# Performance work log

Hardware: AMD Instinct MI355X
Metric: run time of the kernel (lower is better)

The kernel has to match this reference:

```python
import jax, jax.numpy as jnp
import numpy as np

D_MODEL = 1024
N_HEAD = 16
D_HEAD = D_MODEL // N_HEAD
B, S = 4, 2048


def setup_inputs() -> dict:
    key = jax.random.key(0)
    ks = jax.random.split(key, 10)
    def xavier(k, shape):
        fan_in, fan_out = shape[1], shape[0]
        limit = np.sqrt(6.0 / (fan_in + fan_out))
        return jax.random.uniform(k, shape, jnp.float32, -limit, limit)
    x = jax.random.normal(ks[0], (B, S, D_MODEL), jnp.float32)
    mask = jnp.tril(jnp.ones((S, S), jnp.int32))[None, None]  # causal [1,1,S,S]
    return {
        "x": x,
        "Wq": xavier(ks[1], (D_MODEL, D_MODEL)), "bq": jnp.zeros((D_MODEL,), jnp.float32),
        "Wk": xavier(ks[2], (D_MODEL, D_MODEL)), "bk": jnp.zeros((D_MODEL,), jnp.float32),
        "Wv": xavier(ks[3], (D_MODEL, D_MODEL)), "bv": jnp.zeros((D_MODEL,), jnp.float32),
        "Wo": xavier(ks[4], (D_MODEL, D_MODEL)), "bo": jnp.zeros((D_MODEL,), jnp.float32),
        "mask": mask,
    }


def reference(x, Wq, bq, Wk, bk, Wv, bv, Wo, bo, mask):
    b, s, d = x.shape
    # Linear layers use y = x @ W.T + b (torch convention)
    def proj(W, bias):
        y = jnp.einsum('bsd,ed->bse', x, W) + bias
        return y.reshape(b, s, N_HEAD, D_HEAD).transpose(0, 2, 1, 3)  # [B,H,S,Dh]
    q = proj(Wq, bq)
    k = proj(Wk, bk)
    v = proj(Wv, bv)
    scores = jnp.einsum('bhqd,bhkd->bhqk', q, k) / jnp.sqrt(jnp.float32(D_HEAD))
    scores = jnp.where(mask == 0, jnp.float32(-1e9), scores)
    attn = jax.nn.softmax(scores, axis=-1)  # dropout is identity at eval
    context = jnp.einsum('bhqk,bhkd->bhqd', attn, v)
    context = context.transpose(0, 2, 1, 3).reshape(b, s, d)
    return jnp.einsum('bsd,ed->bse', context, Wo) + bo
```

## Files before the change

### kernel.cpp

```cpp
#include <hip/hip_runtime.h>
#include <stdint.h>

#define D_MODEL 1024
#define NHEAD   16
#define DHEAD   64
#define BATCH   4
#define SEQ     2048
#define MTOT    (BATCH*SEQ)

typedef __attribute__((ext_vector_type(4))) float f32x4;
typedef __attribute__((ext_vector_type(8))) short bf16x8;

typedef __attribute__((address_space(3))) uint32_t lds_u32;
typedef const __attribute__((address_space(1))) uint32_t glb_u32;

__device__ static inline void gload_lds16(const void* g, void* l) {
    __builtin_amdgcn_global_load_lds((glb_u32*)g, (lds_u32*)l, 16, 0, 0);
}

__device__ static inline ushort f2bf(float f) {
    uint32_t u = __builtin_bit_cast(uint32_t, f);
    u += 0x7fffu + ((u >> 16) & 1u);
    return (ushort)(u >> 16);
}

__device__ static inline float exp2_fast(float x) {
    float r; asm("v_exp_f32 %0, %1" : "=v"(r) : "v"(x)); return r;
}
__device__ static inline uint32_t cvt_pk_bf16(float a, float b) {
    uint32_t r;
    asm("v_cvt_pk_bf16_f32 %0, %1, %2" : "=v"(r) : "v"(a), "v"(b));
    return r;
}

__global__ __launch_bounds__(256) void convert_kernel(
    const float4* __restrict__ x,
    const float4* __restrict__ wq, const float4* __restrict__ wk,
    const float4* __restrict__ wv, const float4* __restrict__ wo,
    ushort4* __restrict__ xb, ushort4* __restrict__ wb)
{
    const int NX4 = (MTOT * D_MODEL) / 4;
    const int NW4 = (D_MODEL * D_MODEL) / 4;
    const int TOT = NX4 + 4 * NW4;
    for (int i = blockIdx.x * blockDim.x + threadIdx.x; i < TOT;
         i += gridDim.x * blockDim.x) {
        float4 v; ushort4* dst;
        if (i < NX4) { v = x[i]; dst = &xb[i]; }
        else {
            int j = i - NX4;
            int w = j >> 18;
            int r = j & (NW4 - 1);
            const float4* s = (w == 0) ? wq : (w == 1) ? wk : (w == 2) ? wv : wo;
            v = s[r]; dst = &wb[(size_t)w * NW4 + r];
        }
        ushort4 o;
        o.x = f2bf(v.x); o.y = f2bf(v.y); o.z = f2bf(v.z); o.w = f2bf(v.w);
        *dst = o;
    }
}


#define GSWZ(r) ((((r) >> 2) ^ (r)) & 3)

#define GEMM_PIPE_BODY(APTR, BPTR)                                          \
    __shared__ __align__(16) ushort S[4 * 2 * 4096]; \
    const int tid = threadIdx.x;                                            \
    const int w = tid >> 6, l = tid & 63, lo = l & 15, hi = l >> 4;         \
    const int wr = w >> 1, wc = w & 1;                                      \
    const int srow = l >> 2, gg = l & 3;                                    \
    const int r0 = w * 16 + srow, r1 = 64 + w * 16 + srow;                  \
    const int q0 = gg ^ GSWZ(r0), q1 = gg ^ GSWZ(r1);                       \
    const ushort* aS0 = (APTR) + (size_t)(m0 + r0) * 1024 + q0 * 8;         \
    const ushort* aS1 = (APTR) + (size_t)(m0 + r1) * 1024 + q1 * 8;         \
    const ushort* bS0 = (BPTR) + (size_t)(n0 + r0) * 1024 + q0 * 8;         \
    const ushort* bS1 = (BPTR) + (size_t)(n0 + r1) * 1024 + q1 * 8;         \
    const int ldsA0 = (w * 16) * 32, ldsA1 = (64 + w * 16) * 32;            \
    int offA[4], offB[4];                                                   \
    _Pragma("unroll")                                                       \
    for (int mi = 0; mi < 4; ++mi) {                                        \
        const int rA = wr * 64 + mi * 16 + lo;                              \
        offA[mi] = rA * 64 + ((hi ^ GSWZ(rA)) << 4);                        \
        const int rB = wc * 64 + mi * 16 + lo;                              \
        offB[mi] = rB * 64 + ((hi ^ GSWZ(rB)) << 4);                        \
    }                                                                       \
    f32x4 acc[4][4] = {};                                                   \
    auto stage = [&](int st, int t) {                                       \
        ushort* b = &S[st * 8192];                                          \
        const int ko = t * 32;                                              \
        gload_lds16(aS0 + ko, b + ldsA0);                                   \
        gload_lds16(aS1 + ko, b + ldsA1);                                   \
        gload_lds16(bS0 + ko, b + 4096 + ldsA0);                            \
        gload_lds16(bS1 + ko, b + 4096 + ldsA1);                            \
    };                                                                      \
    stage(0, 0); stage(1, 1); stage(2, 2);                                  \
    asm volatile("s_waitcnt vmcnt(8)" ::: "memory");                        \
    __builtin_amdgcn_s_barrier();                                           \
    __builtin_amdgcn_sched_barrier(0);                                      \
    int st = 0;                                                             \
    for (int t = 0; t < 32; ++t) {                                          \
        if (t + 3 < 32) stage((st + 3) & 3, t + 3);                         \
        const char* base = (const char*)&S[st * 8192];                      \
        bf16x8 af[4], bfr[4];                                               \
        _Pragma("unroll")                                                   \
        for (int mi = 0; mi < 4; ++mi) {                                    \
            af[mi]  = *(const bf16x8*)(base + offA[mi]);                    \
            bfr[mi] = *(const bf16x8*)(base + 8192 + offB[mi]);             \
        }                                                                   \
        asm volatile("s_waitcnt lgkmcnt(0)" ::: "memory");                  \
        __builtin_amdgcn_sched_barrier(0);                                  \
        __builtin_amdgcn_s_setprio(1);                                      \
        _Pragma("unroll")                                                   \
        for (int mi = 0; mi < 4; ++mi)                                      \
            _Pragma("unroll")                                               \
            for (int ni = 0; ni < 4; ++ni)                                  \
                acc[mi][ni] = __builtin_amdgcn_mfma_f32_16x16x32_bf16(      \
                    af[mi], bfr[ni], acc[mi][ni], 0, 0, 0);                 \
        __builtin_amdgcn_s_setprio(0);                                      \
        if (t + 3 < 32)      { asm volatile("s_waitcnt vmcnt(8)" ::: "memory"); } \
        else if (t == 29)    { asm volatile("s_waitcnt vmcnt(4)" ::: "memory"); } \
        else if (t == 30)    { asm volatile("s_waitcnt vmcnt(0)" ::: "memory"); } \
        __builtin_amdgcn_s_barrier();                                       \
        __builtin_amdgcn_sched_barrier(0);                                  \
        st = (st + 1) & 3;                                                  \
    }

__global__ __launch_bounds__(256) void gemm_qkv(
    const ushort* __restrict__ A,
    const ushort* __restrict__ W3,
    const float* __restrict__ bq, const float* __restrict__ bk,
    const float* __restrict__ bv,
    ushort* __restrict__ Qb, ushort* __restrict__ Kb, ushort* __restrict__ Vtb,
    float qscale)
{
    const int id = blockIdx.x;
    const int mb = ((id & 7) << 3) | ((id >> 3) & 7);
    const int nb = id >> 6;
    const int m0 = mb * 128, n0 = nb * 128;

    GEMM_PIPE_BODY(A, W3)

    const int region = nb >> 3;
    const float scale = (region == 0) ? qscale : 1.0f;
    const float* bias = (region == 0) ? bq : (region == 1) ? bk : bv;
    ushort* outQK = (region == 0) ? Qb : Kb;

#pragma unroll
    for (int mi = 0; mi < 4; ++mi) {
#pragma unroll
        for (int ni = 0; ni < 4; ++ni) {
            const int gj  = n0 + wc * 64 + ni * 16 + lo;
            const int lcl = gj & 1023;
            const int h = lcl >> 6, dh = lcl & 63;
            const float bj = bias[lcl];
            if (region < 2) {
#pragma unroll
                for (int r = 0; r < 4; ++r) {
                    const int gi = m0 + wr * 64 + mi * 16 + hi * 4 + r;
                    const int b = gi >> 11, s = gi & (SEQ - 1);
                    outQK[(((size_t)(b * NHEAD + h)) * SEQ + s) * DHEAD + dh] =
                        f2bf((acc[mi][ni][r] + bj) * scale);
                }
            } else {
                const int gi0 = m0 + wr * 64 + mi * 16 + hi * 4;
                const int b = gi0 >> 11, s = gi0 & (SEQ - 1);
                ushort4 o4;
                o4.x = f2bf(acc[mi][ni][0] + bj);
                o4.y = f2bf(acc[mi][ni][1] + bj);
                o4.z = f2bf(acc[mi][ni][2] + bj);
                o4.w = f2bf(acc[mi][ni][3] + bj);
                *(ushort4*)&Vtb[(((size_t)(b * NHEAD + h)) * DHEAD + dh) * SEQ + s] = o4;
            }
        }
    }
}

__global__ __launch_bounds__(256) void gemm_out(
    const ushort* __restrict__ A,
    const ushort* __restrict__ W,
    const float*  __restrict__ bias,
    float* __restrict__ out)
{
    const int id = blockIdx.x;
    const int mb = ((id & 7) << 3) | ((id >> 3) & 7);
    const int nb = id >> 6;
    const int m0 = mb * 128, n0 = nb * 128;

    GEMM_PIPE_BODY(A, W)

#pragma unroll
    for (int mi = 0; mi < 4; ++mi)
#pragma unroll
        for (int ni = 0; ni < 4; ++ni) {
            const int gj = n0 + wc * 64 + ni * 16 + lo;
            const float bj = bias[gj];
#pragma unroll
            for (int r = 0; r < 4; ++r) {
                const int gi = m0 + wr * 64 + mi * 16 + hi * 4 + r;
                out[(size_t)gi * D_MODEL + gj] = acc[mi][ni][r] + bj;
            }
        }
}

__global__ __launch_bounds__(256) void attn_kernel(
    const ushort* __restrict__ Q, const ushort* __restrict__ K,
    const ushort* __restrict__ Vt, ushort* __restrict__ ctx)
{
    __shared__ __align__(16) ushort Ks[64 * 64];
    __shared__ __align__(16) ushort Vs[64 * 64];
    __shared__ __align__(16) ushort Pq[4 * 32 * 64];

    const int tid = threadIdx.x;
    const int w = tid >> 6, l = tid & 63, lo = l & 15, hi = l >> 4;
    const int sw = lo & 7;

    const int fid = blockIdx.x;
    const int xcd = fid & 7;
    const int u = fid >> 3;
    const int g = xcd * 8 + (u & 7);
    const int b = g >> 4, h = g & 15;
    const int j = u >> 3;
    const size_t base = (size_t)(b * NHEAD + h) * SEQ * DHEAD;

    const int krow = tid >> 3;
    const int kcol = (tid & 7) * 8;
    char* PqW = (char*)&Pq[w * 2048];

    for (int pass = 0; pass < 2; ++pass) {
        const int qt = pass ? (15 - j) : j;
        const int q0 = qt << 7;
        const int qw0 = q0 + w * 32;

        bf16x8 qf[2][2];
#pragma unroll
        for (int mi = 0; mi < 2; ++mi)
#pragma unroll
            for (int ks = 0; ks < 2; ++ks)
                qf[mi][ks] = *(const bf16x8*)&Q[base +
                    (size_t)(qw0 + mi * 16 + lo) * DHEAD + ks * 32 + hi * 8];

        f32x4 o[2][4] = {};
        float mrow[2] = {-1e30f, -1e30f}, lrow[2] = {0.f, 0.f};

        const int ntiles = (q0 + 128) >> 6;

        bf16x8 kregA[2], vregA[2], kregB[2], vregB[2];
#pragma unroll
        for (int c = 0; c < 2; ++c) {
            kregA[c] = *(const bf16x8*)&K[base + (size_t)(c * 32 + krow) * DHEAD + kcol];
            vregA[c] = *(const bf16x8*)&Vt[base + (size_t)(c * 32 + krow) * SEQ + kcol];
            kregB[c] = *(const bf16x8*)&K[base + (size_t)(64 + c * 32 + krow) * DHEAD + kcol];
            vregB[c] = *(const bf16x8*)&Vt[base + (size_t)(c * 32 + krow) * SEQ + 64 + kcol];
        }

        auto tile_body = [&](int t, bf16x8 (&KR)[2], bf16x8 (&VR)[2]) {
            const int kv0 = t << 6;
            __syncthreads();
#pragma unroll
            for (int c = 0; c < 2; ++c) {
                const int row = c * 32 + krow;
                const int g16 = (tid & 7) ^ (row & 7);
                *(bf16x8*)((char*)Ks + row * 128 + (g16 << 4)) = KR[c];
                *(bf16x8*)((char*)Vs + row * 128 + (g16 << 4)) = VR[c];
            }
            __syncthreads();
            if (t + 2 < ntiles) {
                const int nv0 = kv0 + 128;
#pragma unroll
                for (int c = 0; c < 2; ++c) {
                    KR[c] = *(const bf16x8*)&K[base + (size_t)(nv0 + c * 32 + krow) * DHEAD + kcol];
                    VR[c] = *(const bf16x8*)&Vt[base + (size_t)(c * 32 + krow) * SEQ + nv0 + kcol];
                }
            }
            if (kv0 > qw0 + 31) return;

            f32x4 s[2][4] = {};
            __builtin_amdgcn_s_setprio(1);
#pragma unroll
            for (int ks = 0; ks < 2; ++ks) {
                bf16x8 kf[4];
#pragma unroll
                for (int nj = 0; nj < 4; ++nj)
                    kf[nj] = *(const bf16x8*)((char*)Ks + (nj * 16 + lo) * 128 +
                                              ((((ks << 2) + hi) ^ sw) << 4));
#pragma unroll
                for (int mi = 0; mi < 2; ++mi)
#pragma unroll
                    for (int nj = 0; nj < 4; ++nj)
                        s[mi][nj] = __builtin_amdgcn_mfma_f32_16x16x32_bf16(
                            kf[nj], qf[mi][ks], s[mi][nj], 0, 0, 0);
            }
            __builtin_amdgcn_s_setprio(0);

            if (kv0 + 63 > qw0) {
#pragma unroll
                for (int mi = 0; mi < 2; ++mi) {
                    const int gq = qw0 + mi * 16 + lo;
#pragma unroll
                    for (int nj = 0; nj < 4; ++nj)
#pragma unroll
                        for (int r = 0; r < 4; ++r) {
                            const int gk = kv0 + nj * 16 + hi * 4 + r;
                            if (gk > gq) s[mi][nj][r] = -1e30f;
                        }
                }
            }

            float tl[2], corr[2];
#pragma unroll
            for (int mi = 0; mi < 2; ++mi) {
                float m = s[mi][0][0];
#pragma unroll
                for (int nj = 0; nj < 4; ++nj)
#pragma unroll
                    for (int r = 0; r < 4; ++r) m = fmaxf(m, s[mi][nj][r]);
                tl[mi] = m;
            }
            const bool grow = (tl[0] > mrow[0] + 8.f) | (tl[1] > mrow[1] + 8.f);
            if (__any(grow)) {
#pragma unroll
                for (int mi = 0; mi < 2; ++mi) {
                    float m2 = fmaxf(tl[mi], __shfl_xor(tl[mi], 16));
                    m2 = fmaxf(m2, __shfl_xor(m2, 32));
                    const float mn = fmaxf(mrow[mi], m2);
                    corr[mi] = exp2_fast(mrow[mi] - mn);
                    mrow[mi] = mn;
                }
#pragma unroll
                for (int mi = 0; mi < 2; ++mi)
#pragma unroll
                    for (int r = 0; r < 4; ++r) {
                        const float cb = __shfl(corr[mi], hi * 4 + r);
#pragma unroll
                        for (int ni = 0; ni < 4; ++ni) o[mi][ni][r] *= cb;
                    }
            } else { corr[0] = 1.f; corr[1] = 1.f; }

#pragma unroll
            for (int mi = 0; mi < 2; ++mi) {
                float ls = 0.f;
#pragma unroll
                for (int nj = 0; nj < 4; ++nj) {
#pragma unroll
                    for (int r = 0; r < 4; ++r) {
                        const float p = exp2_fast(s[mi][nj][r] - mrow[mi]);
                        s[mi][nj][r] = p;
                        ls += p;
                    }
                    uint2 pp;
                    pp.x = cvt_pk_bf16(s[mi][nj][0], s[mi][nj][1]);
                    pp.y = cvt_pk_bf16(s[mi][nj][2], s[mi][nj][3]);
                    const int gP = ((nj << 1) + (hi >> 1)) ^ sw;
                    *(uint2*)(PqW + (mi * 16 + lo) * 128 + (gP << 4) + ((hi & 1) << 3)) = pp;
                }
                ls += __shfl_xor(ls, 16);
                ls += __shfl_xor(ls, 32);
                lrow[mi] = lrow[mi] * corr[mi] + ls;
            }

            __builtin_amdgcn_s_setprio(1);
#pragma unroll
            for (int ks2 = 0; ks2 < 2; ++ks2) {
                bf16x8 pf[2], vf[4];
#pragma unroll
                for (int mi = 0; mi < 2; ++mi)
                    pf[mi] = *(const bf16x8*)(PqW + (mi * 16 + lo) * 128 +
                                              ((((ks2 << 2) + hi) ^ sw) << 4));
#pragma unroll
                for (int ni = 0; ni < 4; ++ni)
                    vf[ni] = *(const bf16x8*)((char*)Vs + (ni * 16 + lo) * 128 +
                                              ((((ks2 << 2) + hi) ^ sw) << 4));
#pragma unroll
                for (int mi = 0; mi < 2; ++mi)
#pragma unroll
                    for (int ni = 0; ni < 4; ++ni)
                        o[mi][ni] = __builtin_amdgcn_mfma_f32_16x16x32_bf16(
                            pf[mi], vf[ni], o[mi][ni], 0, 0, 0);
            }
            __builtin_amdgcn_s_setprio(0);
        };

        for (int tt = 0; tt < ntiles; tt += 2) {
            tile_body(tt,     kregA, vregA);
            tile_body(tt + 1, kregB, vregB);
        }

#pragma unroll
        for (int mi = 0; mi < 2; ++mi) {
            const float rv = 1.0f / lrow[mi];
#pragma unroll
            for (int r = 0; r < 4; ++r) {
                const float rb = __shfl(rv, hi * 4 + r);
                const int gq = qw0 + mi * 16 + hi * 4 + r;
#pragma unroll
                for (int ni = 0; ni < 4; ++ni)
                    ctx[((size_t)(b * SEQ + gq)) * D_MODEL + h * DHEAD + ni * 16 + lo] =
                        f2bf(o[mi][ni][r] * rb);
            }
        }
    }
}

extern "C" void kernel_launch(void* const* d_in, const int* in_sizes, int n_in,
                              void* d_out, int out_size, void* d_ws, size_t ws_size,
                              hipStream_t stream) {
    const float* x  = (const float*)d_in[0];
    const float* Wq = (const float*)d_in[1];
    const float* bq = (const float*)d_in[2];
    const float* Wk = (const float*)d_in[3];
    const float* bk = (const float*)d_in[4];
    const float* Wv = (const float*)d_in[5];
    const float* bv = (const float*)d_in[6];
    const float* Wo = (const float*)d_in[7];
    const float* bo = (const float*)d_in[8];

    char* ws = (char*)d_ws;
    ushort* xb  = (ushort*)(ws);
    ushort* wb  = (ushort*)(ws + (16u << 20));
    ushort* Qb  = (ushort*)(ws + (24u << 20));
    ushort* Kb  = (ushort*)(ws + (40u << 20));
    ushort* Vtb = (ushort*)(ws + (56u << 20));
    ushort* ctx = (ushort*)(ws + (72u << 20));

    convert_kernel<<<2048, 256, 0, stream>>>(
        (const float4*)x, (const float4*)Wq, (const float4*)Wk,
        (const float4*)Wv, (const float4*)Wo, (ushort4*)xb, (ushort4*)wb);

    const int NW = D_MODEL * D_MODEL;
    const float qscale = 0.125f * 1.44269504f;

    gemm_qkv<<<1536, 256, 0, stream>>>(xb, wb, bq, bk, bv, Qb, Kb, Vtb, qscale);

    attn_kernel<<<512, 256, 0, stream>>>(Qb, Kb, Vtb, ctx);

    gemm_out<<<512, 256, 0, stream>>>(ctx, wb + 3 * NW, bo, (float*)d_out);
}
```

Measured before the change: 171.4 us.

## Switch projection GEMMs to 32x32x16 MFMA with three-stage LDS pipeline

Replaces the 16x16x32 bf16 MFMA tiling in the QKV and output GEMMs with 32x32x16 MFMA (2x2 tiles of 32x32 per wave, two k-substeps per 32-wide k slice). The LDS ring drops from four stages to three, which halves prefetch depth and frees shared memory, and the final barrier is skipped. Epilogue index math is rewritten for the 32x32 accumulator layout. The larger MFMA shape aims for higher matrix throughput and fewer LDS fragment loads per flop, at the risk of exposing more global-load latency with the shallower pipeline.

```diff
diff --git a/kernel.cpp b/kernel.cpp
--- a/kernel.cpp
+++ b/kernel.cpp
@@ -8,8 +8,9 @@
 #define SEQ     2048
 #define MTOT    (BATCH*SEQ)
 
-typedef __attribute__((ext_vector_type(4))) float f32x4;
-typedef __attribute__((ext_vector_type(8))) short bf16x8;
+typedef __attribute__((ext_vector_type(4)))  float f32x4;
+typedef __attribute__((ext_vector_type(16))) float f32x16;
+typedef __attribute__((ext_vector_type(8)))  short bf16x8;
 
 typedef __attribute__((address_space(3))) uint32_t lds_u32;
 typedef const __attribute__((address_space(1))) uint32_t glb_u32;
@@ -63,65 +64,76 @@
 #define GSWZ(r) ((((r) >> 2) ^ (r)) & 3)
 
 #define GEMM_PIPE_BODY(APTR, BPTR)                                          \
-    __shared__ __align__(16) ushort S[4 * 2 * 4096]; \
+    __shared__ __align__(16) ushort S[3 * 2 * 4096]; \
     const int tid = threadIdx.x;                                            \
-    const int w = tid >> 6, l = tid & 63, lo = l & 15, hi = l >> 4;         \
+    const int w = tid >> 6, l = tid & 63;                                   \
+    const int lo32 = l & 31, hi2 = l >> 5;                                  \
     const int wr = w >> 1, wc = w & 1;                                      \
     const int srow = l >> 2, gg = l & 3;                                    \
     const int r0 = w * 16 + srow, r1 = 64 + w * 16 + srow;                  \
-    const int q0 = gg ^ GSWZ(r0), q1 = gg ^ GSWZ(r1);                       \
-    const ushort* aS0 = (APTR) + (size_t)(m0 + r0) * 1024 + q0 * 8;         \
-    const ushort* aS1 = (APTR) + (size_t)(m0 + r1) * 1024 + q1 * 8;         \
-    const ushort* bS0 = (BPTR) + (size_t)(n0 + r0) * 1024 + q0 * 8;         \
-    const ushort* bS1 = (BPTR) + (size_t)(n0 + r1) * 1024 + q1 * 8;         \
+    const int sq0 = gg ^ GSWZ(r0), sq1 = gg ^ GSWZ(r1);                     \
+    const ushort* aS0 = (APTR) + (size_t)(m0 + r0) * 1024 + sq0 * 8;        \
+    const ushort* aS1 = (APTR) + (size_t)(m0 + r1) * 1024 + sq1 * 8;        \
+    const ushort* bS0 = (BPTR) + (size_t)(n0 + r0) * 1024 + sq0 * 8;        \
+    const ushort* bS1 = (BPTR) + (size_t)(n0 + r1) * 1024 + sq1 * 8;        \
     const int ldsA0 = (w * 16) * 32, ldsA1 = (64 + w * 16) * 32;            \
-    int offA[4], offB[4];                                                   \
+    int offA[2][2], offB[2][2];                                             \
     _Pragma("unroll")                                                       \
-    for (int mi = 0; mi < 4; ++mi) {                                        \
-        const int rA = wr * 64 + mi * 16 + lo;                              \
-        offA[mi] = rA * 64 + ((hi ^ GSWZ(rA)) << 4);                        \
-        const int rB = wc * 64 + mi * 16 + lo;                              \
-        offB[mi] = rB * 64 + ((hi ^ GSWZ(rB)) << 4);                        \
-    }                                                                       \
-    f32x4 acc[4][4] = {};                                                   \
-    auto stage = [&](int st, int t) {                                       \
-        ushort* b = &S[st * 8192];                                          \
-        const int ko = t * 32;                                              \
-        gload_lds16(aS0 + ko, b + ldsA0);                                   \
-        gload_lds16(aS1 + ko, b + ldsA1);                                   \
-        gload_lds16(bS0 + ko, b + 4096 + ldsA0);                            \
-        gload_lds16(bS1 + ko, b + 4096 + ldsA1);                            \
+    for (int mi = 0; mi < 2; ++mi)                                          \
+        _Pragma("unroll")                                                   \
+        for (int ks = 0; ks < 2; ++ks) {                                    \
+            const int rA = wr * 64 + mi * 32 + lo32;                        \
+            offA[mi][ks] = rA * 64 + (((ks * 2 + hi2) ^ GSWZ(rA)) << 4);    \
+            const int rB = wc * 64 + mi * 32 + lo32;                        \
+            offB[mi][ks] = rB * 64 + (((ks * 2 + hi2) ^ GSWZ(rB)) << 4);    \
+        }                                                                   \
+    f32x16 acc[2][2] = {};                                                  \
+    auto stage = [&](int st_, int t_) {                                     \
+        ushort* bp = &S[st_ * 8192];                                        \
+        const int ko = t_ * 32;                                             \
+        gload_lds16(aS0 + ko, bp + ldsA0);                                  \
+        gload_lds16(aS1 + ko, bp + ldsA1);                                  \
+        gload_lds16(bS0 + ko, bp + 4096 + ldsA0);                           \
+        gload_lds16(bS1 + ko, bp + 4096 + ldsA1);                           \
     };                                                                      \
-    stage(0, 0); stage(1, 1); stage(2, 2);                                  \
-    asm volatile("s_waitcnt vmcnt(8)" ::: "memory");                        \
+    stage(0, 0); stage(1, 1);                                               \
+    asm volatile("s_waitcnt vmcnt(4)" ::: "memory");                        \
     __builtin_amdgcn_s_barrier();                                           \
     __builtin_amdgcn_sched_barrier(0);                                      \
     int st = 0;                                                             \
     for (int t = 0; t < 32; ++t) {                                          \
-        if (t + 3 < 32) stage((st + 3) & 3, t + 3);                         \
+        if (t + 2 < 32) {                                                   \
+            int sn = st + 2; if (sn >= 3) sn -= 3;                          \
+            stage(sn, t + 2);                                               \
+        }                                                                   \
         const char* base = (const char*)&S[st * 8192];                      \
-        bf16x8 af[4], bfr[4];                                               \
+        bf16x8 af[2][2], bf[2][2];                                          \
         _Pragma("unroll")                                                   \
-        for (int mi = 0; mi < 4; ++mi) {                                    \
-            af[mi]  = *(const bf16x8*)(base + offA[mi]);                    \
-            bfr[mi] = *(const bf16x8*)(base + 8192 + offB[mi]);             \
-        }                                                                   \
+        for (int mi = 0; mi < 2; ++mi)                                      \
+            _Pragma("unroll")                                               \
+            for (int ks = 0; ks < 2; ++ks) {                                \
+                af[mi][ks] = *(const bf16x8*)(base + offA[mi][ks]);         \
+                bf[mi][ks] = *(const bf16x8*)(base + 8192 + offB[mi][ks]);  \
+            }                                                               \
         asm volatile("s_waitcnt lgkmcnt(0)" ::: "memory");                  \
         __builtin_amdgcn_sched_barrier(0);                                  \
         __builtin_amdgcn_s_setprio(1);                                      \
         _Pragma("unroll")                                                   \
-        for (int mi = 0; mi < 4; ++mi)                                      \
+        for (int ks = 0; ks < 2; ++ks)                                      \
             _Pragma("unroll")                                               \
-            for (int ni = 0; ni < 4; ++ni)                                  \
-                acc[mi][ni] = __builtin_amdgcn_mfma_f32_16x16x32_bf16(      \
-                    af[mi], bfr[ni], acc[mi][ni], 0, 0, 0);                 \
+            for (int mi = 0; mi < 2; ++mi)                                  \
+                _Pragma("unroll")                                           \
+                for (int ni = 0; ni < 2; ++ni)                              \
+                    acc[mi][ni] = __builtin_amdgcn_mfma_f32_32x32x16_bf16(  \
+                        af[mi][ks], bf[ni][ks], acc[mi][ni], 0, 0, 0);      \
         __builtin_amdgcn_s_setprio(0);                                      \
-        if (t + 3 < 32)      { asm volatile("s_waitcnt vmcnt(8)" ::: "memory"); } \
-        else if (t == 29)    { asm volatile("s_waitcnt vmcnt(4)" ::: "memory"); } \
-        else if (t == 30)    { asm volatile("s_waitcnt vmcnt(0)" ::: "memory"); } \
-        __builtin_amdgcn_s_barrier();                                       \
-        __builtin_amdgcn_sched_barrier(0);                                  \
-        st = (st + 1) & 3;                                                  \
+        if (t + 2 < 32)   { asm volatile("s_waitcnt vmcnt(4)" ::: "memory"); } \
+        else if (t == 30) { asm volatile("s_waitcnt vmcnt(0)" ::: "memory"); } \
+        if (t < 31) {                                                       \
+            __builtin_amdgcn_s_barrier();                                   \
+            __builtin_amdgcn_sched_barrier(0);                              \
+        }                                                                   \
+        ++st; if (st >= 3) st = 0;                                          \
     }
 
 __global__ __launch_bounds__(256) void gemm_qkv(
@@ -145,30 +157,30 @@
     ushort* outQK = (region == 0) ? Qb : Kb;
 
 #pragma unroll
-    for (int mi = 0; mi < 4; ++mi) {
-#pragma unroll
-        for (int ni = 0; ni < 4; ++ni) {
-            const int gj  = n0 + wc * 64 + ni * 16 + lo;
+    for (int mi = 0; mi < 2; ++mi) {
+#pragma unroll
+        for (int ni = 0; ni < 2; ++ni) {
+            const int gj  = n0 + wc * 64 + ni * 32 + lo32;
             const int lcl = gj & 1023;
             const int h = lcl >> 6, dh = lcl & 63;
             const float bj = bias[lcl];
-            if (region < 2) {
-#pragma unroll
-                for (int r = 0; r < 4; ++r) {
-                    const int gi = m0 + wr * 64 + mi * 16 + hi * 4 + r;
-                    const int b = gi >> 11, s = gi & (SEQ - 1);
-                    outQK[(((size_t)(b * NHEAD + h)) * SEQ + s) * DHEAD + dh] =
-                        f2bf((acc[mi][ni][r] + bj) * scale);
+#pragma unroll
+            for (int rq = 0; rq < 4; ++rq) {
+                const int gi0 = m0 + wr * 64 + mi * 32 + 8 * rq + 4 * hi2;
+                const int b = gi0 >> 11, s0 = gi0 & (SEQ - 1);
+                if (region < 2) {
+#pragma unroll
+                    for (int rr = 0; rr < 4; ++rr)
+                        outQK[(((size_t)(b * NHEAD + h)) * SEQ + s0 + rr) * DHEAD + dh] =
+                            f2bf((acc[mi][ni][rq * 4 + rr] + bj) * scale);
+                } else {
+                    ushort4 o4;
+                    o4.x = f2bf(acc[mi][ni][rq * 4 + 0] + bj);
+                    o4.y = f2bf(acc[mi][ni][rq * 4 + 1] + bj);
+                    o4.z = f2bf(acc[mi][ni][rq * 4 + 2] + bj);
+                    o4.w = f2bf(acc[mi][ni][rq * 4 + 3] + bj);
+                    *(ushort4*)&Vtb[(((size_t)(b * NHEAD + h)) * DHEAD + dh) * SEQ + s0] = o4;
                 }
-            } else {
-                const int gi0 = m0 + wr * 64 + mi * 16 + hi * 4;
-                const int b = gi0 >> 11, s = gi0 & (SEQ - 1);
-                ushort4 o4;
-                o4.x = f2bf(acc[mi][ni][0] + bj);
-                o4.y = f2bf(acc[mi][ni][1] + bj);
-                o4.z = f2bf(acc[mi][ni][2] + bj);
-                o4.w = f2bf(acc[mi][ni][3] + bj);
-                *(ushort4*)&Vtb[(((size_t)(b * NHEAD + h)) * DHEAD + dh) * SEQ + s] = o4;
             }
         }
     }
@@ -188,15 +200,18 @@
     GEMM_PIPE_BODY(A, W)
 
 #pragma unroll
-    for (int mi = 0; mi < 4; ++mi)
-#pragma unroll
-        for (int ni = 0; ni < 4; ++ni) {
-            const int gj = n0 + wc * 64 + ni * 16 + lo;
+    for (int mi = 0; mi < 2; ++mi)
+#pragma unroll
+        for (int ni = 0; ni < 2; ++ni) {
+            const int gj = n0 + wc * 64 + ni * 32 + lo32;
             const float bj = bias[gj];
 #pragma unroll
-            for (int r = 0; r < 4; ++r) {
-                const int gi = m0 + wr * 64 + mi * 16 + hi * 4 + r;
-                out[(size_t)gi * D_MODEL + gj] = acc[mi][ni][r] + bj;
+            for (int rq = 0; rq < 4; ++rq) {
+                const int gi0 = m0 + wr * 64 + mi * 32 + 8 * rq + 4 * hi2;
+#pragma unroll
+                for (int rr = 0; rr < 4; ++rr)
+                    out[(size_t)(gi0 + rr) * D_MODEL + gj] =
+                        acc[mi][ni][rq * 4 + rr] + bj;
             }
         }
 }
```

Result: no change. 170.5 us (-0.5%).

## Rewrite projection GEMMs with 256x128 tiles, 8 waves, and 3-stage BK=64 pipeline

Applied to the files above, without the earlier changes.

Replaces the 128x128, 4-wave, BK=32 four-stage GEMM body with a 256x128 tile computed by 8 waves (512 threads), a BK=64 K step, and a three-buffer LDS pipeline. The global-to-LDS loads are interleaved across four compute phases per K step, and the LDS layout uses an XOR swizzle over 8 chunks. Block-to-XCD mapping is changed so each XCD handles a contiguous range of M blocks. The aim is more operand reuse per load, fewer barriers per FLOP, and better L2 locality. In exchange, grids are smaller (768 and 256 blocks), occupancy is one block per CU with 144KB of LDS, and there are more barriers inside each K step.

```diff
diff --git a/kernel.cpp b/kernel.cpp
--- a/kernel.cpp
+++ b/kernel.cpp
@@ -8,8 +8,8 @@
 #define SEQ     2048
 #define MTOT    (BATCH*SEQ)
 
-typedef __attribute__((ext_vector_type(4))) float f32x4;
-typedef __attribute__((ext_vector_type(8))) short bf16x8;
+typedef __attribute__((ext_vector_type(4)))  float f32x4;
+typedef __attribute__((ext_vector_type(8)))  short bf16x8;
 
 typedef __attribute__((address_space(3))) uint32_t lds_u32;
 typedef const __attribute__((address_space(1))) uint32_t glb_u32;
@@ -60,71 +60,95 @@
 }
 
 
-#define GSWZ(r) ((((r) >> 2) ^ (r)) & 3)
-
-#define GEMM_PIPE_BODY(APTR, BPTR)                                          \
-    __shared__ __align__(16) ushort S[4 * 2 * 4096]; \
+#define GEMM8_BODY(APTR, BPTR, NKT)                                         \
+    __shared__ __align__(16) ushort S[3 * 24576];  \
     const int tid = threadIdx.x;                                            \
-    const int w = tid >> 6, l = tid & 63, lo = l & 15, hi = l >> 4;         \
-    const int wr = w >> 1, wc = w & 1;                                      \
-    const int srow = l >> 2, gg = l & 3;                                    \
-    const int r0 = w * 16 + srow, r1 = 64 + w * 16 + srow;                  \
-    const int q0 = gg ^ GSWZ(r0), q1 = gg ^ GSWZ(r1);                       \
-    const ushort* aS0 = (APTR) + (size_t)(m0 + r0) * 1024 + q0 * 8;         \
-    const ushort* aS1 = (APTR) + (size_t)(m0 + r1) * 1024 + q1 * 8;         \
-    const ushort* bS0 = (BPTR) + (size_t)(n0 + r0) * 1024 + q0 * 8;         \
-    const ushort* bS1 = (BPTR) + (size_t)(n0 + r1) * 1024 + q1 * 8;         \
-    const int ldsA0 = (w * 16) * 32, ldsA1 = (64 + w * 16) * 32;            \
-    int offA[4], offB[4];                                                   \
-    _Pragma("unroll")                                                       \
-    for (int mi = 0; mi < 4; ++mi) {                                        \
-        const int rA = wr * 64 + mi * 16 + lo;                              \
-        offA[mi] = rA * 64 + ((hi ^ GSWZ(rA)) << 4);                        \
-        const int rB = wc * 64 + mi * 16 + lo;                              \
-        offB[mi] = rB * 64 + ((hi ^ GSWZ(rB)) << 4);                        \
-    }                                                                       \
+    const int w = tid >> 6, l = tid & 63;                                   \
+    const int lo = l & 15, hi = l >> 4;                        \
+    const int wm = w >> 1, wn = w & 1;                                      \
+    const int srA = w * 8 + (l >> 3);                 \
+    const int sgA = l & 7;                             \
     f32x4 acc[4][4] = {};                                                   \
-    auto stage = [&](int st, int t) {                                       \
-        ushort* b = &S[st * 8192];                                          \
-        const int ko = t * 32;                                              \
-        gload_lds16(aS0 + ko, b + ldsA0);                                   \
-        gload_lds16(aS1 + ko, b + ldsA1);                                   \
-        gload_lds16(bS0 + ko, b + 4096 + ldsA0);                            \
-        gload_lds16(bS1 + ko, b + 4096 + ldsA1);                            \
+    auto stageA2 = [&](int buf, int kt, int j0) {                           \
+        ushort* SA = &S[buf * 24576];                                       \
+        _Pragma("unroll")                                                   \
+        for (int j = j0; j < j0 + 2; ++j) {                                 \
+            const int row = j * 64 + srA;                                   \
+            const int g = sgA ^ (row & 7);                                  \
+            gload_lds16((APTR) + (size_t)(m0 + row) * 1024 + kt * 64 + g * 8,\
+                        SA + (j * 64 + w * 8) * 64);                        \
+        }                                                                   \
     };                                                                      \
-    stage(0, 0); stage(1, 1); stage(2, 2);                                  \
-    asm volatile("s_waitcnt vmcnt(8)" ::: "memory");                        \
+    auto stageB2 = [&](int buf, int kt) {                                   \
+        ushort* SB = &S[buf * 24576] + 16384;                               \
+        _Pragma("unroll")                                                   \
+        for (int j = 0; j < 2; ++j) {                                       \
+            const int row = j * 64 + srA;                                   \
+            const int g = sgA ^ (row & 7);                                  \
+            gload_lds16((BPTR) + (size_t)(n0 + row) * 1024 + kt * 64 + g * 8,\
+                        SB + (j * 64 + w * 8) * 64);                        \
+        }                                                                   \
+    };                                                                      \
+             \
+    stageA2(0, 0, 0); stageA2(0, 0, 2); stageB2(0, 0);                      \
+    stageA2(1, 1, 0); stageA2(1, 1, 2); stageB2(1, 1);                      \
+    asm volatile("s_waitcnt vmcnt(6)" ::: "memory");                        \
     __builtin_amdgcn_s_barrier();                                           \
     __builtin_amdgcn_sched_barrier(0);                                      \
-    int st = 0;                                                             \
-    for (int t = 0; t < 32; ++t) {                                          \
-        if (t + 3 < 32) stage((st + 3) & 3, t + 3);                         \
-        const char* base = (const char*)&S[st * 8192];                      \
-        bf16x8 af[4], bfr[4];                                               \
+    int cur = 0;                                                            \
+    for (int kt = 0; kt < (NKT); ++kt) {                                    \
+        const int stg = (cur + 2 >= 3) ? cur - 1 : cur + 2;                 \
+        const char* SA = (const char*)&S[cur * 24576];                      \
+        const char* SB = SA + 32768;                                        \
+        const bool doStage = (kt + 2 < (NKT));                              \
         _Pragma("unroll")                                                   \
-        for (int mi = 0; mi < 4; ++mi) {                                    \
-            af[mi]  = *(const bf16x8*)(base + offA[mi]);                    \
-            bfr[mi] = *(const bf16x8*)(base + 8192 + offB[mi]);             \
+        for (int p = 0; p < 4; ++p) {                                       \
+            bf16x8 af[2][2], bf[2][2];                                      \
+            _Pragma("unroll")                                               \
+            for (int mi = 0; mi < 2; ++mi)                                  \
+                _Pragma("unroll")                                           \
+                for (int ks = 0; ks < 2; ++ks) {                            \
+                    const int ar = wm * 64 + (p >> 1) * 32 + mi * 16 + lo;  \
+                    const int ga = (ks * 4 + hi) ^ (ar & 7);                \
+                    af[mi][ks] = *(const bf16x8*)(SA + ar * 128 + ga * 16); \
+                    const int bc = wn * 64 + (p & 1) * 32 + mi * 16 + lo;   \
+                    const int gb = (ks * 4 + hi) ^ (bc & 7);                \
+                    bf[mi][ks] = *(const bf16x8*)(SB + bc * 128 + gb * 16); \
+                }                                                           \
+            if (doStage) {                                                  \
+                if (p == 0)      stageA2(stg, kt + 2, 0);                   \
+                else if (p == 1) stageA2(stg, kt + 2, 2);                   \
+                else if (p == 2) stageB2(stg, kt + 2);                      \
+            }                                                               \
+            __builtin_amdgcn_s_barrier();                                   \
+            asm volatile("s_waitcnt lgkmcnt(0)" ::: "memory");              \
+            __builtin_amdgcn_sched_barrier(0);                              \
+            __builtin_amdgcn_s_setprio(1);                                  \
+            _Pragma("unroll")                                               \
+            for (int ks = 0; ks < 2; ++ks)                                  \
+                _Pragma("unroll")                                           \
+                for (int mi = 0; mi < 2; ++mi)                              \
+                    _Pragma("unroll")                                       \
+                    for (int ni = 0; ni < 2; ++ni)                          \
+                        acc[(p >> 1) * 2 + mi][(p & 1) * 2 + ni] =          \
+                            __builtin_amdgcn_mfma_f32_16x16x32_bf16(        \
+                                af[mi][ks], bf[ni][ks],                     \
+                                acc[(p >> 1) * 2 + mi][(p & 1) * 2 + ni],   \
+                                0, 0, 0);                                   \
+            __builtin_amdgcn_s_setprio(0);                                  \
+            if (p == 3) {                                                   \
+                if (kt + 2 < (NKT))                                         \
+                    { asm volatile("s_waitcnt vmcnt(6)" ::: "memory"); }    \
+                else if (kt + 2 == (NKT))                                   \
+                    { asm volatile("s_waitcnt vmcnt(0)" ::: "memory"); }    \
+            }                                                               \
+            __builtin_amdgcn_s_barrier();                                   \
+            __builtin_amdgcn_sched_barrier(0);                              \
         }                                                                   \
-        asm volatile("s_waitcnt lgkmcnt(0)" ::: "memory");                  \
-        __builtin_amdgcn_sched_barrier(0);                                  \
-        __builtin_amdgcn_s_setprio(1);                                      \
-        _Pragma("unroll")                                                   \
-        for (int mi = 0; mi < 4; ++mi)                                      \
-            _Pragma("unroll")                                               \
-            for (int ni = 0; ni < 4; ++ni)                                  \
-                acc[mi][ni] = __builtin_amdgcn_mfma_f32_16x16x32_bf16(      \
-                    af[mi], bfr[ni], acc[mi][ni], 0, 0, 0);                 \
-        __builtin_amdgcn_s_setprio(0);                                      \
-        if (t + 3 < 32)      { asm volatile("s_waitcnt vmcnt(8)" ::: "memory"); } \
-        else if (t == 29)    { asm volatile("s_waitcnt vmcnt(4)" ::: "memory"); } \
-        else if (t == 30)    { asm volatile("s_waitcnt vmcnt(0)" ::: "memory"); } \
-        __builtin_amdgcn_s_barrier();                                       \
-        __builtin_amdgcn_sched_barrier(0);                                  \
-        st = (st + 1) & 3;                                                  \
+        cur = (cur == 2) ? 0 : cur + 1;                                     \
     }
 
-__global__ __launch_bounds__(256) void gemm_qkv(
+__global__ __launch_bounds__(512, 1) void gemm_qkv(
     const ushort* __restrict__ A,
     const ushort* __restrict__ W3,
     const float* __restrict__ bq, const float* __restrict__ bk,
@@ -133,11 +157,12 @@
     float qscale)
 {
     const int id = blockIdx.x;
-    const int mb = ((id & 7) << 3) | ((id >> 3) & 7);
-    const int nb = id >> 6;
-    const int m0 = mb * 128, n0 = nb * 128;
-
-    GEMM_PIPE_BODY(A, W3)
+    const int xcd = id & 7, q = id >> 3;
+    const int mb = xcd * 4 + (q & 3);
+    const int nb = q >> 2;
+    const int m0 = mb * 256, n0 = nb * 128;
+
+    GEMM8_BODY(A, W3, 16)
 
     const int region = nb >> 3;
     const float scale = (region == 0) ? qscale : 1.0f;
@@ -148,56 +173,53 @@
     for (int mi = 0; mi < 4; ++mi) {
 #pragma unroll
         for (int ni = 0; ni < 4; ++ni) {
-            const int gj  = n0 + wc * 64 + ni * 16 + lo;
+            const int gj  = n0 + wn * 64 + ni * 16 + lo;
             const int lcl = gj & 1023;
             const int h = lcl >> 6, dh = lcl & 63;
             const float bj = bias[lcl];
+            const int gi0 = m0 + wm * 64 + mi * 16 + hi * 4;
+            const int b = gi0 >> 11, s0 = gi0 & (SEQ - 1);
             if (region < 2) {
 #pragma unroll
-                for (int r = 0; r < 4; ++r) {
-                    const int gi = m0 + wr * 64 + mi * 16 + hi * 4 + r;
-                    const int b = gi >> 11, s = gi & (SEQ - 1);
-                    outQK[(((size_t)(b * NHEAD + h)) * SEQ + s) * DHEAD + dh] =
+                for (int r = 0; r < 4; ++r)
+                    outQK[(((size_t)(b * NHEAD + h)) * SEQ + s0 + r) * DHEAD + dh] =
                         f2bf((acc[mi][ni][r] + bj) * scale);
-                }
             } else {
-                const int gi0 = m0 + wr * 64 + mi * 16 + hi * 4;
-                const int b = gi0 >> 11, s = gi0 & (SEQ - 1);
                 ushort4 o4;
                 o4.x = f2bf(acc[mi][ni][0] + bj);
                 o4.y = f2bf(acc[mi][ni][1] + bj);
                 o4.z = f2bf(acc[mi][ni][2] + bj);
                 o4.w = f2bf(acc[mi][ni][3] + bj);
-                *(ushort4*)&Vtb[(((size_t)(b * NHEAD + h)) * DHEAD + dh) * SEQ + s] = o4;
+                *(ushort4*)&Vtb[(((size_t)(b * NHEAD + h)) * DHEAD + dh) * SEQ + s0] = o4;
             }
         }
     }
 }
 
-__global__ __launch_bounds__(256) void gemm_out(
+__global__ __launch_bounds__(512, 1) void gemm_out(
     const ushort* __restrict__ A,
     const ushort* __restrict__ W,
     const float*  __restrict__ bias,
     float* __restrict__ out)
 {
     const int id = blockIdx.x;
-    const int mb = ((id & 7) << 3) | ((id >> 3) & 7);
-    const int nb = id >> 6;
-    const int m0 = mb * 128, n0 = nb * 128;
-
-    GEMM_PIPE_BODY(A, W)
+    const int xcd = id & 7, q = id >> 3;
+    const int mb = xcd * 4 + (q & 3);
+    const int nb = q >> 2;
+    const int m0 = mb * 256, n0 = nb * 128;
+
+    GEMM8_BODY(A, W, 16)
 
 #pragma unroll
     for (int mi = 0; mi < 4; ++mi)
 #pragma unroll
         for (int ni = 0; ni < 4; ++ni) {
-            const int gj = n0 + wc * 64 + ni * 16 + lo;
+            const int gj = n0 + wn * 64 + ni * 16 + lo;
             const float bj = bias[gj];
-#pragma unroll
-            for (int r = 0; r < 4; ++r) {
-                const int gi = m0 + wr * 64 + mi * 16 + hi * 4 + r;
-                out[(size_t)gi * D_MODEL + gj] = acc[mi][ni][r] + bj;
-            }
+            const int gi0 = m0 + wm * 64 + mi * 16 + hi * 4;
+#pragma unroll
+            for (int r = 0; r < 4; ++r)
+                out[(size_t)(gi0 + r) * D_MODEL + gj] = acc[mi][ni][r] + bj;
         }
 }
 
@@ -428,9 +450,9 @@
     const int NW = D_MODEL * D_MODEL;
     const float qscale = 0.125f * 1.44269504f;
 
-    gemm_qkv<<<1536, 256, 0, stream>>>(xb, wb, bq, bk, bv, Qb, Kb, Vtb, qscale);
+    gemm_qkv<<<768, 512, 0, stream>>>(xb, wb, bq, bk, bv, Qb, Kb, Vtb, qscale);
 
     attn_kernel<<<512, 256, 0, stream>>>(Qb, Kb, Vtb, ctx);
 
-    gemm_out<<<512, 256, 0, stream>>>(ctx, wb + 3 * NW, bo, (float*)d_out);
-}
+    gemm_out<<<256, 512, 0, stream>>>(ctx, wb + 3 * NW, bo, (float*)d_out);
+}
```

After: 179.3 us. 1.05x slower.
